# Kernel tuning notes

Hardware: AMD Instinct MI355X
Metric: run time of the kernel (lower is better)

The kernel has to match this reference:

```python
import jax, jax.numpy as jnp
import numpy as np

IN_FEATURES = 4096
OUT_FEATURES = 11008
GROUP_SIZE = 128
NUM_GROUPS = IN_FEATURES // GROUP_SIZE  # 32
BATCH, SEQ = 4, 2048


def setup_inputs() -> dict:
    key = jax.random.key(0)
    k_in, k_w, k_s, k_b = jax.random.split(key, 4)
    inp = jax.random.normal(k_in, (BATCH, SEQ, IN_FEATURES), dtype=jnp.float32)
    # 4-bit symmetric codes in [-8, 8)
    weight = jax.random.randint(k_w, (OUT_FEATURES, NUM_GROUPS, GROUP_SIZE), -8, 8, dtype=jnp.int32)
    # small positive per-group scales, as produced by quantization calibration
    scales = jax.random.uniform(k_s, (OUT_FEATURES, NUM_GROUPS), dtype=jnp.float32) * 0.02 + 1e-4
    bias = jax.random.normal(k_b, (OUT_FEATURES,), dtype=jnp.float32)
    return {"input": inp, "weight": weight, "scales": scales, "bias": bias}


def reference(input, weight, scales, bias):
    # Fused dequant-matmul: symmetric weight-only quantization.
    # weight: [O, G, gs] int codes; scales: [O, G] per-group scale.
    O, G, gs = weight.shape
    W = weight.astype(jnp.float32) * scales[:, :, None]   # [O, G, gs] dequantized
    W = W.reshape(O, G * gs)                               # [O, in_features]
    out = jnp.einsum('bsi,oi->bso', input, W)              # [B, S, O]
    return out + bias
```

## Files before the change

### kernel.cpp

```cpp
#include <hip/hip_runtime.h>
#include <hip/hip_bf16.h>
#include <cstdint>

#define M_DIM 8192
#define K_DIM 4096
#define N_DIM 11008
#define NGROUPS 32

typedef __attribute__((ext_vector_type(4))) float f32x4;
typedef __attribute__((ext_vector_type(4))) int i32x4;
typedef __attribute__((ext_vector_type(8))) __bf16 bf16x8;

__device__ __forceinline__ unsigned int f2bf(float f) {
  unsigned int u = __builtin_bit_cast(unsigned int, f);
  return (u + 0x7FFFu + ((u >> 16) & 1u)) >> 16;
}
__device__ __forceinline__ unsigned int pk2(float lo, float hi) {
  return f2bf(lo) | (f2bf(hi) << 16);
}

__global__ __launch_bounds__(256) void quantA_kernel(const float* __restrict__ in,
                                                     char* __restrict__ outA,
                                                     float* __restrict__ sA) {
  const int row = blockIdx.x * 4 + (threadIdx.x >> 6);
  const int lane = threadIdx.x & 63;
  const float* p = in + (size_t)row * K_DIM;
  float mx = 0.f;
#pragma unroll
  for (int e = 0; e < 16; ++e) {
    float4 v = *(const float4*)(p + e * 256 + lane * 4);
    mx = fmaxf(mx, fmaxf(fmaxf(fabsf(v.x), fabsf(v.y)), fmaxf(fabsf(v.z), fabsf(v.w))));
  }
#pragma unroll
  for (int off = 32; off; off >>= 1) mx = fmaxf(mx, __shfl_xor(mx, off));
  mx = fmaxf(mx, 1e-30f);
  const float rq = 127.f / mx;
  if (lane == 0) sA[row] = mx / 127.f;
  char* op = outA + (size_t)row * K_DIM;
#pragma unroll
  for (int e = 0; e < 16; ++e) {
    float4 v = *(const float4*)(p + e * 256 + lane * 4);
    unsigned pk = ((unsigned)((int)rintf(v.x * rq)) & 0xFFu)
                | (((unsigned)((int)rintf(v.y * rq)) & 0xFFu) << 8)
                | (((unsigned)((int)rintf(v.z * rq)) & 0xFFu) << 16)
                | (((unsigned)((int)rintf(v.w * rq)) & 0xFFu) << 24);
    *(unsigned*)(op + e * 256 + lane * 4) = pk;
  }
}

__global__ __launch_bounds__(256) void quantW_kernel(const int* __restrict__ wc,
                                                     const float* __restrict__ sc,
                                                     char* __restrict__ outB,
                                                     float* __restrict__ sW) {
  const int col = blockIdx.x * 4 + (threadIdx.x >> 6);
  const int lane = threadIdx.x & 63;
  const int4* p = (const int4*)(wc + (size_t)col * K_DIM);
  const float* scp = sc + col * NGROUPS;
  float mx = 0.f;
#pragma unroll
  for (int e = 0; e < 16; ++e) {
    int4 c = p[e * 64 + lane];
    float s = scp[e * 2 + (lane >> 5)];
    float m = fmaxf(fmaxf(fabsf((float)c.x), fabsf((float)c.y)),
                    fmaxf(fabsf((float)c.z), fabsf((float)c.w)));
    mx = fmaxf(mx, m * s);
  }
#pragma unroll
  for (int off = 32; off; off >>= 1) mx = fmaxf(mx, __shfl_xor(mx, off));
  mx = fmaxf(mx, 1e-30f);
  const float rq = 127.f / mx;
  if (lane == 0) sW[col] = mx / 127.f;
  char* op = outB + (size_t)col * K_DIM;
#pragma unroll
  for (int e = 0; e < 16; ++e) {
    int4 c = p[e * 64 + lane];
    float s = scp[e * 2 + (lane >> 5)] * rq;
    unsigned pk = ((unsigned)((int)rintf((float)c.x * s)) & 0xFFu)
                | (((unsigned)((int)rintf((float)c.y * s)) & 0xFFu) << 8)
                | (((unsigned)((int)rintf((float)c.z * s)) & 0xFFu) << 16)
                | (((unsigned)((int)rintf((float)c.w * s)) & 0xFFu) << 24);
    *(unsigned*)(op + e * 256 + lane * 4) = pk;
  }
}

__device__ __forceinline__ void gload16(const void* g, void* l) {
  __builtin_amdgcn_global_load_lds((const __attribute__((address_space(1))) void*)g,
                                   (__attribute__((address_space(3))) void*)l,
                                   16, 0, 0);
}

#define BM 256
#define BN 256
#define BKB 64
#define NKT (K_DIM / BKB)
#define TILES_M (M_DIM / BM)
#define TILES_N (N_DIM / BN)
#define NB2 (TILES_M * TILES_N)
#define TSZ (BM * BKB)

#define VMCNT_(n) asm volatile("s_waitcnt vmcnt(" #n ")" ::: "memory")
#define VMCNT(n) VMCNT_(n)
#define BAR() __builtin_amdgcn_s_barrier()

__global__ __launch_bounds__(512, 2) void gemmq_kernel(
    const char* __restrict__ A,
    const char* __restrict__ B,
    const float* __restrict__ sA,
    const float* __restrict__ sW,
    const float* __restrict__ bias,
    float* __restrict__ out) {
  __shared__ __align__(16) char lA[4][TSZ];
  __shared__ __align__(16) char lB[4][TSZ];

  const int t = threadIdx.x;
  const int bid = blockIdx.x;
  const int wg = (bid & 7) * (NB2 / 8) + (bid >> 3);
  const int m0 = (wg / TILES_N) * BM;
  const int n0 = (wg % TILES_N) * BN;

  const int w = t >> 6;
  const int lane = t & 63;
  const int wm = w >> 2;
  const int wn = w & 3;

  const int r0 = w * 32 + (lane >> 2);
  const int r1 = r0 + 16;
  const int pgs = lane & 3;
  const size_t aoff0 = (size_t)(m0 + r0) * K_DIM + (unsigned)(pgs ^ ((r0 >> 1) & 3)) * 16;
  const size_t aoff1 = (size_t)(m0 + r1) * K_DIM + (unsigned)(pgs ^ ((r1 >> 1) & 3)) * 16;
  const size_t boff0 = (size_t)(n0 + r0) * K_DIM + (unsigned)(pgs ^ ((r0 >> 1) & 3)) * 16;
  const size_t boff1 = (size_t)(n0 + r1) * K_DIM + (unsigned)(pgs ^ ((r1 >> 1) & 3)) * 16;
  const int ld0 = w * 2048;
  const int ld1 = w * 2048 + 1024;

  i32x4 acc[8][4];
#pragma unroll
  for (int i = 0; i < 8; ++i)
#pragma unroll
    for (int j = 0; j < 4; ++j) {
      i32x4 z = {0, 0, 0, 0};
      acc[i][j] = z;
    }

#define STAGE(buf, kt)                                                        \
  do {                                                                        \
    gload16(A + aoff0 + (size_t)(kt) * BKB, &lA[buf][ld0]);                   \
    gload16(A + aoff1 + (size_t)(kt) * BKB, &lA[buf][ld1]);                   \
    gload16(B + boff0 + (size_t)(kt) * BKB, &lB[buf][ld0]);                   \
    gload16(B + boff1 + (size_t)(kt) * BKB, &lB[buf][ld1]);                   \
  } while (0)

#define TILE_CORE(CB)                                                         \
  i32x4 af[8], bq[4];                                                         \
  _Pragma("unroll") for (int i = 0; i < 8; ++i) {                             \
    const int row = wm * 128 + i * 16 + (lane & 15);                          \
    const int pg = (lane >> 4) ^ ((row >> 1) & 3);                            \
    af[i] = *(const i32x4*)&lA[CB][row * 64 + pg * 16];                       \
  }                                                                           \
  _Pragma("unroll") for (int j = 0; j < 4; ++j) {                             \
    const int row = wn * 64 + j * 16 + (lane & 15);                           \
    const int pg = (lane >> 4) ^ ((row >> 1) & 3);                            \
    bq[j] = *(const i32x4*)&lB[CB][row * 64 + pg * 16];                       \
  }

#define TILE_MMA()                                                            \
  __builtin_amdgcn_s_setprio(1);                                              \
  _Pragma("unroll") for (int i = 0; i < 8; ++i)                               \
  _Pragma("unroll") for (int j = 0; j < 4; ++j)                               \
    acc[i][j] = __builtin_amdgcn_mfma_i32_16x16x64_i8(af[i], bq[j],           \
                                                      acc[i][j], 0, 0, 0);    \
  __builtin_amdgcn_s_setprio(0);

#define TILE(CB, SB, KT3, VN)                                                 \
  {                                                                           \
    TILE_CORE(CB)                                                             \
    STAGE(SB, KT3);                                                           \
    TILE_MMA()                                                                \
    VMCNT(VN);                                                                \
    BAR();                                                                    \
  }
#define TILE_NS(CB, VN)                                                       \
  {                                                                           \
    TILE_CORE(CB)                                                             \
    TILE_MMA()                                                                \
    VMCNT(VN);                                                                \
    BAR();                                                                    \
  }

  STAGE(0, 0);
  STAGE(1, 1);
  STAGE(2, 2);
  VMCNT(8);
  BAR();

  for (int it = 0; it < 15; ++it) {
    const int k = it * 4;
    TILE(0, 3, k + 3, 8)
    TILE(1, 0, k + 4, 8)
    TILE(2, 1, k + 5, 8)
    TILE(3, 2, k + 6, 8)
  }
  TILE(0, 3, 63, 8)
  TILE_NS(1, 4)
  TILE_NS(2, 0)
  {
    TILE_CORE(3)
    TILE_MMA()
  }

  const int colb = n0 + wn * 64 + (lane & 15);
  const int rowb = m0 + wm * 128 + ((lane >> 4) << 2);
  float sar[8][4];
#pragma unroll
  for (int ai = 0; ai < 8; ++ai)
#pragma unroll
    for (int r = 0; r < 4; ++r)
      sar[ai][r] = sA[rowb + ai * 16 + r];
#pragma unroll
  for (int j = 0; j < 4; ++j) {
    const int col = colb + j * 16;
    const float sc2 = sW[col];
    const float bv = bias[col];
#pragma unroll
    for (int ai = 0; ai < 8; ++ai) {
      const int row = rowb + ai * 16;
#pragma unroll
      for (int r = 0; r < 4; ++r)
        out[(size_t)(row + r) * N_DIM + col] =
            (float)acc[ai][j][r] * sar[ai][r] * sc2 + bv;
    }
  }
#undef STAGE
#undef TILE_CORE
#undef TILE_MMA
#undef TILE
#undef TILE_NS
}

#define FBM 128
#define FBN 128
#define FBK 64
#define FNT_N 86
#define FNT_M 64
#define FNB (FNT_N * FNT_M)

__global__ __launch_bounds__(256, 2) void gemm_fb_kernel(
    const float* __restrict__ Ain, const int* __restrict__ Wcodes,
    const float* __restrict__ scales, const float* __restrict__ bias,
    float* __restrict__ out) {
  __shared__ unsigned short lsA[FBM * FBK];
  __shared__ unsigned short lsB[FBN * FBK];

  const int t = threadIdx.x;
  const int bid = blockIdx.x;
  const int wg = (bid & 7) * (FNB / 8) + (bid >> 3);
  const int m0 = (wg / FNT_N) * FBM;
  const int n0 = (wg % FNT_N) * FBN;

  const int w = t >> 6;
  const int lane = t & 63;
  const int wm = w >> 1, wn = w & 1;
  const int srow = t >> 3;
  const int sp = t & 7;
  const int skc = sp ^ (srow & 7);

  f32x4 acc[4][4];
#pragma unroll
  for (int i = 0; i < 4; ++i)
#pragma unroll
    for (int j = 0; j < 4; ++j) {
      f32x4 z = {0.f, 0.f, 0.f, 0.f};
      acc[i][j] = z;
    }

  for (int kt = 0; kt < K_DIM / FBK; ++kt) {
    const int kg = kt * FBK + skc * 8;
#pragma unroll
    for (int c = 0; c < 4; ++c) {
      const int arow = m0 + c * 32 + srow;
      const float* ap = Ain + (size_t)arow * K_DIM + kg;
      float4 a0 = *(const float4*)ap;
      float4 a1 = *(const float4*)(ap + 4);
      uint4 va;
      va.x = pk2(a0.x, a0.y); va.y = pk2(a0.z, a0.w);
      va.z = pk2(a1.x, a1.y); va.w = pk2(a1.z, a1.w);
      *(uint4*)&lsA[(c * 32 + srow) * FBK + sp * 8] = va;

      const int nrow = n0 + c * 32 + srow;
      const float s = scales[nrow * NGROUPS + (kg >> 7)];
      const int4* wp = (const int4*)(Wcodes + (size_t)nrow * K_DIM + kg);
      int4 c0 = wp[0], c1 = wp[1];
      uint4 vb;
      vb.x = pk2((float)c0.x * s, (float)c0.y * s);
      vb.y = pk2((float)c0.z * s, (float)c0.w * s);
      vb.z = pk2((float)c1.x * s, (float)c1.y * s);
      vb.w = pk2((float)c1.z * s, (float)c1.w * s);
      *(uint4*)&lsB[(c * 32 + srow) * FBK + sp * 8] = vb;
    }
    __syncthreads();
#pragma unroll
    for (int kk = 0; kk < 2; ++kk) {
      bf16x8 af[4], bfr[4];
#pragma unroll
      for (int i = 0; i < 4; ++i) {
        const int row = wm * 64 + i * 16 + (lane & 15);
        const int pg = (kk * 4 + (lane >> 4)) ^ (row & 7);
        af[i] = *(const bf16x8*)&lsA[row * FBK + pg * 8];
      }
#pragma unroll
      for (int j = 0; j < 4; ++j) {
        const int row = wn * 64 + j * 16 + (lane & 15);
        const int pg = (kk * 4 + (lane >> 4)) ^ (row & 7);
        bfr[j] = *(const bf16x8*)&lsB[row * FBK + pg * 8];
      }
#pragma unroll
      for (int i = 0; i < 4; ++i)
#pragma unroll
        for (int j = 0; j < 4; ++j)
          acc[i][j] = __builtin_amdgcn_mfma_f32_16x16x32_bf16(af[i], bfr[j], acc[i][j], 0, 0, 0);
    }
    __syncthreads();
  }

  const int colb = n0 + wn * 64 + (lane & 15);
  const int rowb = m0 + wm * 64 + ((lane >> 4) << 2);
#pragma unroll
  for (int j = 0; j < 4; ++j) {
    const int col = colb + j * 16;
    const float bv = bias[col];
#pragma unroll
    for (int i = 0; i < 4; ++i) {
      const int row = rowb + i * 16;
#pragma unroll
      for (int r = 0; r < 4; ++r)
        out[(size_t)(row + r) * N_DIM + col] = acc[i][j][r] + bv;
    }
  }
}

extern "C" void kernel_launch(void* const* d_in, const int* in_sizes, int n_in,
                              void* d_out, int out_size, void* d_ws, size_t ws_size,
                              hipStream_t stream) {
  const float* Ain = (const float*)d_in[0];
  const int* Wc = (const int*)d_in[1];
  const float* sc = (const float*)d_in[2];
  const float* bias = (const float*)d_in[3];
  float* out = (float*)d_out;

  const size_t offW = (size_t)M_DIM * K_DIM;
  const size_t offSA = offW + (size_t)N_DIM * K_DIM;
  const size_t offSW = offSA + (size_t)M_DIM * 4;
  const size_t need = offSW + (size_t)N_DIM * 4;

  if (ws_size >= need) {
    char* wsA = (char*)d_ws;
    char* wsB = (char*)d_ws + offW;
    float* sA = (float*)((char*)d_ws + offSA);
    float* sW = (float*)((char*)d_ws + offSW);
    quantA_kernel<<<M_DIM / 4, 256, 0, stream>>>(Ain, wsA, sA);
    quantW_kernel<<<N_DIM / 4, 256, 0, stream>>>(Wc, sc, wsB, sW);
    gemmq_kernel<<<NB2, 512, 0, stream>>>(wsA, wsB, sA, sW, bias, out);
  } else {
    gemm_fb_kernel<<<FNB, 256, 0, stream>>>(Ain, Wc, sc, bias, out);
  }
}
```

Before: 522.5 us.

## Double K tile depth and switch to double-buffered LDS pipeline

Doubles the K depth per LDS tile from 64 to 128 bytes and cuts buffering from four stages to two, halving the number of barriers per K. Each tile is consumed as two 64-byte chunks and the next tile is prefetched while the first chunk runs. The LDS swizzle is reworked to an 8-way XOR for the wider rows. The trade-off is a shallower prefetch: with vmcnt(0) at every tile, global latency is hidden by only one tile of compute, and this may expose load stalls.

```diff
diff --git a/kernel.cpp b/kernel.cpp
--- a/kernel.cpp
+++ b/kernel.cpp
@@ -91,7 +91,7 @@
 
 #define BM 256
 #define BN 256
-#define BKB 64
+#define BKB 128
 #define NKT (K_DIM / BKB)
 #define TILES_M (M_DIM / BM)
 #define TILES_N (N_DIM / BN)
@@ -109,8 +109,8 @@
     const float* __restrict__ sW,
     const float* __restrict__ bias,
     float* __restrict__ out) {
-  __shared__ __align__(16) char lA[4][TSZ];
-  __shared__ __align__(16) char lB[4][TSZ];
+  __shared__ __align__(16) char lA[2][TSZ];
+  __shared__ __align__(16) char lB[2][TSZ];
 
   const int t = threadIdx.x;
   const int bid = blockIdx.x;
@@ -123,15 +123,17 @@
   const int wm = w >> 2;
   const int wn = w & 3;
 
-  const int r0 = w * 32 + (lane >> 2);
-  const int r1 = r0 + 16;
-  const int pgs = lane & 3;
-  const size_t aoff0 = (size_t)(m0 + r0) * K_DIM + (unsigned)(pgs ^ ((r0 >> 1) & 3)) * 16;
-  const size_t aoff1 = (size_t)(m0 + r1) * K_DIM + (unsigned)(pgs ^ ((r1 >> 1) & 3)) * 16;
-  const size_t boff0 = (size_t)(n0 + r0) * K_DIM + (unsigned)(pgs ^ ((r0 >> 1) & 3)) * 16;
-  const size_t boff1 = (size_t)(n0 + r1) * K_DIM + (unsigned)(pgs ^ ((r1 >> 1) & 3)) * 16;
-  const int ld0 = w * 2048;
-  const int ld1 = w * 2048 + 1024;
+  const int srow8 = t >> 3;
+  const int pg8 = t & 7;
+  size_t aoffs[4], boffs[4];
+#pragma unroll
+  for (int c = 0; c < 4; ++c) {
+    const int row = c * 64 + srow8;
+    const unsigned sg = (unsigned)(pg8 ^ (row & 7));
+    aoffs[c] = (size_t)(m0 + row) * K_DIM + sg * 16;
+    boffs[c] = (size_t)(n0 + row) * K_DIM + sg * 16;
+  }
+  const int ldb = w * 1024;
 
   i32x4 acc[8][4];
 #pragma unroll
@@ -144,26 +146,25 @@
 
 #define STAGE(buf, kt)                                                        \
   do {                                                                        \
-    gload16(A + aoff0 + (size_t)(kt) * BKB, &lA[buf][ld0]);                   \
-    gload16(A + aoff1 + (size_t)(kt) * BKB, &lA[buf][ld1]);                   \
-    gload16(B + boff0 + (size_t)(kt) * BKB, &lB[buf][ld0]);                   \
-    gload16(B + boff1 + (size_t)(kt) * BKB, &lB[buf][ld1]);                   \
+    _Pragma("unroll") for (int c = 0; c < 4; ++c) {                           \
+      gload16(A + aoffs[c] + (size_t)(kt) * BKB, &lA[buf][c * 8192 + ldb]);   \
+      gload16(B + boffs[c] + (size_t)(kt) * BKB, &lB[buf][c * 8192 + ldb]);   \
+    }                                                                         \
   } while (0)
 
-#define TILE_CORE(CB)                                                         \
-  i32x4 af[8], bq[4];                                                         \
+#define READ_CHUNK(CB, h, af, bq)                                             \
   _Pragma("unroll") for (int i = 0; i < 8; ++i) {                             \
     const int row = wm * 128 + i * 16 + (lane & 15);                          \
-    const int pg = (lane >> 4) ^ ((row >> 1) & 3);                            \
-    af[i] = *(const i32x4*)&lA[CB][row * 64 + pg * 16];                       \
+    const int pg = ((h) * 4 + (lane >> 4)) ^ (row & 7);                       \
+    af[i] = *(const i32x4*)&lA[CB][row * BKB + pg * 16];                      \
   }                                                                           \
   _Pragma("unroll") for (int j = 0; j < 4; ++j) {                             \
     const int row = wn * 64 + j * 16 + (lane & 15);                           \
-    const int pg = (lane >> 4) ^ ((row >> 1) & 3);                            \
-    bq[j] = *(const i32x4*)&lB[CB][row * 64 + pg * 16];                       \
-  }
-
-#define TILE_MMA()                                                            \
+    const int pg = ((h) * 4 + (lane >> 4)) ^ (row & 7);                       \
+    bq[j] = *(const i32x4*)&lB[CB][row * BKB + pg * 16];                      \
+  }
+
+#define MMA_CHUNK(af, bq)                                                     \
   __builtin_amdgcn_s_setprio(1);                                              \
   _Pragma("unroll") for (int i = 0; i < 8; ++i)                               \
   _Pragma("unroll") for (int j = 0; j < 4; ++j)                               \
@@ -171,41 +172,35 @@
                                                       acc[i][j], 0, 0, 0);    \
   __builtin_amdgcn_s_setprio(0);
 
-#define TILE(CB, SB, KT3, VN)                                                 \
+#define TILE(CB, NB_, KT)                                                     \
   {                                                                           \
-    TILE_CORE(CB)                                                             \
-    STAGE(SB, KT3);                                                           \
-    TILE_MMA()                                                                \
-    VMCNT(VN);                                                                \
+    i32x4 af0[8], bq0[4];                                                     \
+    READ_CHUNK(CB, 0, af0, bq0)                                               \
+    STAGE(NB_, (KT) + 1);                                                     \
+    MMA_CHUNK(af0, bq0)                                                       \
+    i32x4 af1[8], bq1[4];                                                     \
+    READ_CHUNK(CB, 1, af1, bq1)                                               \
+    MMA_CHUNK(af1, bq1)                                                       \
+    VMCNT(0);                                                                 \
     BAR();                                                                    \
   }
-#define TILE_NS(CB, VN)                                                       \
-  {                                                                           \
-    TILE_CORE(CB)                                                             \
-    TILE_MMA()                                                                \
-    VMCNT(VN);                                                                \
-    BAR();                                                                    \
-  }
 
   STAGE(0, 0);
-  STAGE(1, 1);
-  STAGE(2, 2);
-  VMCNT(8);
+  VMCNT(0);
   BAR();
 
   for (int it = 0; it < 15; ++it) {
-    const int k = it * 4;
-    TILE(0, 3, k + 3, 8)
-    TILE(1, 0, k + 4, 8)
-    TILE(2, 1, k + 5, 8)
-    TILE(3, 2, k + 6, 8)
-  }
-  TILE(0, 3, 63, 8)
-  TILE_NS(1, 4)
-  TILE_NS(2, 0)
+    TILE(0, 1, 2 * it)
+    TILE(1, 0, 2 * it + 1)
+  }
+  TILE(0, 1, 30)
   {
-    TILE_CORE(3)
-    TILE_MMA()
+    i32x4 af0[8], bq0[4];
+    READ_CHUNK(1, 0, af0, bq0)
+    MMA_CHUNK(af0, bq0)
+    i32x4 af1[8], bq1[4];
+    READ_CHUNK(1, 1, af1, bq1)
+    MMA_CHUNK(af1, bq1)
   }
 
   const int colb = n0 + wn * 64 + (lane & 15);
@@ -231,10 +226,9 @@
     }
   }
 #undef STAGE
-#undef TILE_CORE
-#undef TILE_MMA
+#undef READ_CHUNK
+#undef MMA_CHUNK
 #undef TILE
-#undef TILE_NS
 }
 
 #define FBM 128
```

Measured after the change: 526.6 us. About the same (+0.8%).
